# Performance work log

Measured on AMD Instinct MI355X. Metric: run time of the kernel, lower is better.

The kernel has to match this reference:

```python
import jax, jax.numpy as jnp
import numpy as np

EPS = 1e-12
N_WAY, N_SHOT, C_IN, H_IN, W_IN = 5, 5, 640, 24, 24
TOP_LR = 0.8


def _normalize(x, axis):
    # torch F.normalize: x / max(||x||_2, eps)
    n = jnp.sqrt(jnp.sum(x * x, axis=axis, keepdims=True))
    return x / jnp.maximum(n, EPS)


def _conv1x1(x, W, b):
    # x: (B,C,H,W), W: (O,C), b: (O,)
    return jnp.einsum('bchw,oc->bohw', x, W) + b[None, :, None, None]


def _attlayer(x, Wc, bc, Wq, bq, Wk, bk):
    B, C, H, W = x.shape
    HW = H * W
    n_way, n_shot = N_WAY, N_SHOT
    scale = 1.0 / (C ** 0.5)
    x5 = _conv1x1(x, Wc, bc) + x
    x5 = _conv1x1(x5, Wq, bq)            # note: query_transform applied here
    # query_transform applied AGAIN (faithful to original)
    xq = _conv1x1(x5, Wq, bq).reshape(n_way, n_shot, C, HW)
    x_query = jnp.swapaxes(xq, 2, 3).reshape(n_way, n_shot * HW, C)
    xk = _conv1x1(x5, Wk, bk).reshape(n_way, n_shot, C, HW)
    x_key = jnp.swapaxes(xk, 1, 2).reshape(n_way, C, n_shot * HW)
    x_w1 = jnp.matmul(x_query, x_key) * scale          # (n_way, n_shot*HW, n_shot*HW)
    x_w = x_w1.reshape(n_way, n_shot * HW, n_shot, HW).max(-1).mean(-1)
    x_w = jax.nn.softmax(x_w.reshape(n_way, n_shot, HW), axis=-1)
    norm0 = _normalize(x5, 1).reshape(n_way, n_shot, C, H, W)
    # hard-max mask over spatial positions
    mask = (x_w == x_w.max(-1, keepdims=True)).astype(x.dtype)   # (n_way, n_shot, HW)
    seeds = (norm0 * mask.reshape(n_way, n_shot, 1, H, W)).sum((3, 4))  # (n_way, n_shot, C)
    # conv3d with 1x1 spatial kernel over full channel depth == einsum
    cor = jnp.einsum('nkcyx,okc->noyx', norm0, seeds).reshape(n_way, n_shot, HW)
    cmin = cor.min(-1, keepdims=True)
    cmax = cor.max(-1, keepdims=True)
    cor = (cor - cmin) / (cmax - cmin + EPS)
    cormap = cor.reshape(n_way * n_shot, 1, H, W)
    x51 = (x5 * cormap).reshape(n_way, n_shot, C, H, W)
    return x51.mean((1, 3, 4))  # (n_way, C)


def _cdsnet(lf):
    B, C, H, W = lf.shape
    HW = H * W
    n_way, n_shot = N_WAY, N_SHOT
    lfn = _normalize(lf, 1)
    X = jnp.swapaxes(lfn.reshape(B, C, HW), 1, 2)          # (B, HW, C)
    intra = X.reshape(n_way, n_shot * HW, C)
    # d_intra: masked (1-eye) gram mean == (x_i . S_way - ||x_i||^2)/(n_shot*HW)
    S_way = intra.sum(1)                                    # (n_way, C)
    d_intra = (jnp.einsum('nic,nc->ni', intra, S_way) - (intra * intra).sum(-1)) / (n_shot * HW)
    # d_inter: block-diagonal (same-image) pairs masked out
    S_tot = X.sum((0, 1))                                   # (C,)
    S_img = X.sum(1)                                        # (B, C)
    d_inter = (jnp.einsum('bic,c->bi', X, S_tot) - jnp.einsum('bic,bc->bi', X, S_img)) / (B * HW)
    cds = jax.nn.sigmoid(d_intra.reshape(n_way, -1) / d_inter.reshape(n_way, -1))  # (n_way, n_shot*HW)
    k = int(n_shot * HW * TOP_LR)
    _, sel_idx = jax.lax.top_k(cds, k)
    sel = jnp.zeros((n_way, n_shot * HW), lf.dtype)
    sel = sel.at[jnp.arange(n_way)[:, None], sel_idx].set(1.0)
    pos_small = sel.reshape(n_way * n_shot, 1, H, W)
    slf = lf * pos_small                                    # select_local_features
    slf_n = jnp.swapaxes(_normalize(slf.reshape(B, C, HW), 1), 1, 2)
    slf_n = slf_n.reshape(n_way, n_shot, HW, C)
    m1 = slf_n.reshape(n_way, n_shot * HW, C).mean(1)       # (n_way, C)
    l_intra = jnp.matmul(m1, m1.T) * (1.0 - jnp.eye(n_way, dtype=lf.dtype))
    m2 = slf_n.mean(2)                                      # (n_way, n_shot, C)
    l_inter = jnp.einsum('nsc,ntc->nst', m2, m2) * (1.0 - jnp.eye(n_shot, dtype=lf.dtype))
    loss = jnp.exp(l_inter.mean() / l_intra.mean())
    pos_index = jnp.broadcast_to(pos_small, (B, C, H, W))
    neg_index = 1.0 - pos_index
    return loss, pos_index, neg_index


def setup_inputs() -> dict:
    key = jax.random.key(0)
    ks = jax.random.split(key, 7)
    C = C_IN
    s = N_WAY * N_SHOT
    scale = 1.0 / np.sqrt(C)
    lf = jax.random.normal(ks[0], (s, C, H_IN, W_IN), jnp.float32)
    Wc = jax.random.normal(ks[1], (C, C), jnp.float32) * scale
    bc = jax.random.normal(ks[2], (C,), jnp.float32) * 0.01
    Wq = jax.random.normal(ks[3], (C, C), jnp.float32) * scale
    bq = jax.random.normal(ks[4], (C,), jnp.float32) * 0.01
    Wk = jax.random.normal(ks[5], (C, C), jnp.float32) * scale
    bk = jax.random.normal(ks[6], (C,), jnp.float32) * 0.01
    return {'local_feature': lf, 'Wc': Wc, 'bc': bc, 'Wq': Wq, 'bq': bq, 'Wk': Wk, 'bk': bk}


def reference(local_feature, Wc, bc, Wq, bq, Wk, bk):
    s, c, h, w = local_feature.shape
    hw = h * w
    proto1 = _attlayer(local_feature, Wc, bc, Wq, bq, Wk, bk)   # (n_way, C)
    global_proto = jnp.broadcast_to(proto1[:, None, :], (N_WAY, N_SHOT, c)).reshape(s, c)
    gpa = global_proto[:, None, :]                               # (s, 1, C) -> broadcasts to (s, HW, C)
    contrastive_loss, pos_index, neg_index = _cdsnet(local_feature)
    pos_x = _normalize(jnp.swapaxes((local_feature * pos_index).reshape(s, c, hw), 1, 2), -1)
    neg_x = _normalize(jnp.swapaxes((local_feature * neg_index).reshape(s, c, hw), 1, 2), -1)
    pos_value = jnp.exp(pos_x * gpa).sum(-1).mean(-1).mean(-1)
    neg_value = jnp.exp(neg_x * gpa).sum(-1).mean(-1).mean(-1)
    ctc_loss = -jnp.log(pos_value / neg_value)
    return (contrastive_loss, ctc_loss, pos_index)
```

## Files before the change

kernel.cpp:

```cpp
#include <hip/hip_runtime.h>
#include <math.h>

#define NW 5
#define NS 5
#define BB 25
#define CD 640
#define HWD 576
#define NP 2880
#define KTOP 2304
#define EPSF 1e-12f

typedef __attribute__((ext_vector_type(8))) short short8;
typedef __attribute__((ext_vector_type(4))) float f32x4;

__device__ inline unsigned short f2bf(float x) {
    unsigned u = __float_as_uint(x);
    return (unsigned short)((u + 0x7fffu + ((u >> 16) & 1u)) >> 16);
}
__device__ inline float bf2f(unsigned short h) { return __uint_as_float(((unsigned)h) << 16); }

__device__ inline void gload_lds16(const void* g, void* l) {
    __builtin_amdgcn_global_load_lds(
        (const __attribute__((address_space(1))) unsigned int*)g,
        (__attribute__((address_space(3))) unsigned int*)l, 16, 0, 0);
}

__device__ void dev_gemm640(const float* __restrict__ A, const float* __restrict__ B,
                            const float* __restrict__ add, float* __restrict__ C,
                            unsigned short* __restrict__ H, unsigned short* __restrict__ L,
                            int mode, int bx, int by, char* smem)
{
    float (*At)[68] = (float(*)[68])smem;
    float (*Bt)[64] = (float(*)[64])(smem + 8704);
    const int o0 = by * 64, j0 = bx * 64;
    const int t  = threadIdx.x;
    const int to = (t >> 4) * 4, tj = (t & 15) * 4;

    float acc[4][4];
#pragma unroll
    for (int r = 0; r < 4; ++r)
#pragma unroll
        for (int s = 0; s < 4; ++s) acc[r][s] = 0.f;

    for (int c0 = 0; c0 < CD; c0 += 32) {
        __syncthreads();
        {
            const int r = t >> 3, c8 = (t & 7) * 8;
            float4 b0 = *(const float4*)&B[(size_t)(c0+r)*CD + j0 + c8];
            float4 b1 = *(const float4*)&B[(size_t)(c0+r)*CD + j0 + c8 + 4];
            *(float4*)&Bt[r][c8]     = b0;
            *(float4*)&Bt[r][c8 + 4] = b1;
            if (mode == 0) {
                float4 a0 = *(const float4*)&A[(size_t)(c0+r)*CD + o0 + c8];
                float4 a1 = *(const float4*)&A[(size_t)(c0+r)*CD + o0 + c8 + 4];
                *(float4*)&At[r][c8]     = a0;
                *(float4*)&At[r][c8 + 4] = a1;
            } else {
                const int r2 = t >> 2, c82 = (t & 3) * 8;
                float4 a0 = *(const float4*)&A[(size_t)(o0+r2)*CD + c0 + c82];
                float4 a1 = *(const float4*)&A[(size_t)(o0+r2)*CD + c0 + c82 + 4];
                At[c82+0][r2] = a0.x; At[c82+1][r2] = a0.y;
                At[c82+2][r2] = a0.z; At[c82+3][r2] = a0.w;
                At[c82+4][r2] = a1.x; At[c82+5][r2] = a1.y;
                At[c82+6][r2] = a1.z; At[c82+7][r2] = a1.w;
            }
        }
        __syncthreads();
#pragma unroll
        for (int kk = 0; kk < 32; ++kk) {
            float4 av = *(const float4*)&At[kk][to];
            float4 bv = *(const float4*)&Bt[kk][tj];
            float aa[4] = {av.x, av.y, av.z, av.w};
            float bb[4] = {bv.x, bv.y, bv.z, bv.w};
#pragma unroll
            for (int r = 0; r < 4; ++r)
#pragma unroll
                for (int s = 0; s < 4; ++s)
                    acc[r][s] = fmaf(aa[r], bb[s], acc[r][s]);
        }
    }

#pragma unroll
    for (int r = 0; r < 4; ++r) {
        float v[4] = {acc[r][0], acc[r][1], acc[r][2], acc[r][3]};
        const size_t base = (size_t)(o0+to+r)*CD + j0 + tj;
        if (add != nullptr) {
            float4 ad = *(const float4*)&add[base];
            v[0] += ad.x; v[1] += ad.y; v[2] += ad.z; v[3] += ad.w;
        }
        if (C != nullptr) {
            float4 o4; o4.x = v[0]; o4.y = v[1]; o4.z = v[2]; o4.w = v[3];
            *(float4*)&C[base] = o4;
        }
        if (H != nullptr) {
            ushort4 h, l;
            h.x = f2bf(v[0]); h.y = f2bf(v[1]); h.z = f2bf(v[2]); h.w = f2bf(v[3]);
            l.x = f2bf(v[0] - bf2f(h.x)); l.y = f2bf(v[1] - bf2f(h.y));
            l.z = f2bf(v[2] - bf2f(h.z)); l.w = f2bf(v[3] - bf2f(h.w));
            *(ushort4*)&H[base] = h; *(ushort4*)&L[base] = l;
        }
    }
}

__device__ void dev_convert(const float* __restrict__ in, unsigned short* __restrict__ Oh,
                            unsigned short* __restrict__ Ol, int b, int xidx, char* smem)
{
    float (*tile)[65] = (float(*)[65])smem;
    const int c0 = (xidx / 9) * 64;
    const int p0 = (xidx % 9) * 64;
    const int t  = threadIdx.x;
    const float* src = in + (size_t)b * CD * HWD;
#pragma unroll
    for (int it = 0; it < 4; ++it) {
        int cl = (t >> 4) + 16*it, pl = (t & 15) * 4;
        float4 v = *(const float4*)&src[(size_t)(c0+cl)*HWD + p0 + pl];
        tile[cl][pl] = v.x; tile[cl][pl+1] = v.y; tile[cl][pl+2] = v.z; tile[cl][pl+3] = v.w;
    }
    __syncthreads();
#pragma unroll
    for (int it = 0; it < 4; ++it) {
        int pl = (t >> 4) + 16*it, clb = (t & 15) * 4;
        ushort4 hv, lv;
        float x0 = tile[clb+0][pl], x1 = tile[clb+1][pl], x2 = tile[clb+2][pl], x3 = tile[clb+3][pl];
        hv.x = f2bf(x0); hv.y = f2bf(x1); hv.z = f2bf(x2); hv.w = f2bf(x3);
        lv.x = f2bf(x0 - bf2f(hv.x)); lv.y = f2bf(x1 - bf2f(hv.y));
        lv.z = f2bf(x2 - bf2f(hv.z)); lv.w = f2bf(x3 - bf2f(hv.w));
        size_t o = (size_t)(b*HWD + p0 + pl) * CD + c0 + clb;
        *(ushort4*)&Oh[o] = hv;
        *(ushort4*)&Ol[o] = lv;
    }
}

__global__ __launch_bounds__(256) void prep_a(
    const float* __restrict__ lf, const float* __restrict__ Wc,
    const float* __restrict__ bc, const float* __restrict__ Wq,
    const float* __restrict__ bq, const float* __restrict__ Wk,
    const float* __restrict__ bk,
    float* __restrict__ M2, float* __restrict__ Weff,
    float* __restrict__ wqtbk, float* __restrict__ bqwk, float* __restrict__ beff,
    float* __restrict__ sbb,
    unsigned short* __restrict__ lfTh, unsigned short* __restrict__ lfTl,
    float* __restrict__ cor, float* __restrict__ sumsq, float* __restrict__ rvsum,
    float* __restrict__ proto1, float* __restrict__ scal)
{
    __shared__ __align__(16) char smem[16896];
    const int blk = blockIdx.x;
    const int t = threadIdx.x;
    if (blk < 100) {
        dev_gemm640(Wq, Wk, nullptr, M2, nullptr, nullptr, 0, blk % 10, blk / 10, smem);
    } else if (blk < 200) {
        int b2 = blk - 100;
        dev_gemm640(Wq, Wc, Wq, Weff, nullptr, nullptr, 1, b2 % 10, b2 / 10, smem);
    } else if (blk < 210) {
        const int o = (blk - 200)*64 + (t >> 2);
        const int m0 = (t & 3) * 160;
        float s1 = 0.f, s2 = 0.f;
        for (int m = m0; m < m0 + 160; ++m) {
            s1 = fmaf(Wq[(size_t)m*CD + o], bk[m], s1);
            s2 = fmaf(bq[m], Wk[(size_t)m*CD + o], s2);
        }
        s1 += __shfl_xor(s1, 1, 64); s1 += __shfl_xor(s1, 2, 64);
        s2 += __shfl_xor(s2, 1, 64); s2 += __shfl_xor(s2, 2, 64);
        if ((t & 3) == 0) { wqtbk[o] = s1; bqwk[o] = s2; }
    } else if (blk < 220) {
        const int o = (blk - 210)*64 + (t >> 2);
        const int m0 = (t & 3) * 160;
        const float* ap = Wq + (size_t)o*CD + m0;
        float a = 0.f;
        for (int m = 0; m < 160; ++m) a = fmaf(ap[m], bc[m0 + m], a);
        a += __shfl_xor(a, 1, 64); a += __shfl_xor(a, 2, 64);
        if ((t & 3) == 0) beff[o] = a + bq[o];
    } else if (blk == 220) {
        __shared__ float red[4];
        float a = 0.f;
        for (int m = t; m < CD; m += 256) a = fmaf(bq[m], bk[m], a);
        for (int off2 = 32; off2; off2 >>= 1) a += __shfl_down(a, off2, 64);
        if ((t & 63) == 0) red[t >> 6] = a;
        __syncthreads();
        if (t == 0) sbb[0] = red[0] + red[1] + red[2] + red[3];
    } else if (blk < 2471) {
        const int idx = blk - 221;
        dev_convert(lf, lfTh, lfTl, idx / 90, idx % 90, smem);
    } else {
        const int i0 = (blk - 2471)*256 + t;
        for (int i = i0; i < 14400; i += 8192) { cor[i] = 0.f; sumsq[i] = 0.f; rvsum[i] = 0.f; }
        for (int i = i0; i < 3200; i += 8192) proto1[i] = 0.f;
        if (i0 < 2) scal[i0] = 0.f;
    }
}

__global__ __launch_bounds__(256) void prep_b(
    const float* __restrict__ M2, const float* __restrict__ Weff,
    const float* __restrict__ beff, const float* __restrict__ wqtbk,
    unsigned short* __restrict__ WeH, unsigned short* __restrict__ WeL,
    unsigned short* __restrict__ MeH, unsigned short* __restrict__ MeL,
    float* __restrict__ wbias)
{
    __shared__ __align__(16) char smem[16896];
    const int blk = blockIdx.x;
    const int t = threadIdx.x;
    if (blk < 100) {
        dev_gemm640(M2, Weff, nullptr, nullptr, MeH, MeL, 1, blk % 10, blk / 10, smem);
    } else if (blk < 200) {
        int i = (blk - 100)*256 + t;
        float4 v = ((const float4*)Weff)[i];
        ushort4 h, l;
        h.x = f2bf(v.x); h.y = f2bf(v.y); h.z = f2bf(v.z); h.w = f2bf(v.w);
        l.x = f2bf(v.x - bf2f(h.x)); l.y = f2bf(v.y - bf2f(h.y));
        l.z = f2bf(v.z - bf2f(h.z)); l.w = f2bf(v.w - bf2f(h.w));
        ((ushort4*)WeH)[i] = h; ((ushort4*)WeL)[i] = l;
    } else {
        const int o = (blk - 200)*64 + (t >> 2);
        const int m0 = (t & 3) * 160;
        const float* ap = M2 + (size_t)o*CD + m0;
        float a = 0.f;
        for (int m = 0; m < 160; ++m) a = fmaf(ap[m], beff[m0 + m], a);
        a += __shfl_xor(a, 1, 64); a += __shfl_xor(a, 2, 64);
        if ((t & 3) == 0) wbias[o] = a + wqtbk[o];
    }
}

__global__ __launch_bounds__(256) void conv2x(
    const unsigned short* __restrict__ Ah_, const unsigned short* __restrict__ Al_,
    const unsigned short* __restrict__ WeH, const unsigned short* __restrict__ WeL,
    const unsigned short* __restrict__ MeH, const unsigned short* __restrict__ MeL,
    const float* __restrict__ beff, const float* __restrict__ wbias,
    const float* __restrict__ bqwk,
    unsigned short* __restrict__ x5h, unsigned short* __restrict__ x5l,
    unsigned short* __restrict__ wh,  unsigned short* __restrict__ wl,
    float* __restrict__ sumsq, float* __restrict__ rvsum)
{
    __shared__ __align__(16) unsigned short lds[14336];
    const int obx  = blockIdx.x;
    const int osel = (obx < 5);
    const int o0   = (osel ? obx : obx - 5) * 128;
    const unsigned short* Wh = osel ? WeH : MeH;
    const unsigned short* Wl = osel ? WeL : MeL;
    const float* bias = osel ? beff : wbias;
    unsigned short* Oh = osel ? x5h : wh;
    unsigned short* Ol = osel ? x5l : wl;
    const int row0 = blockIdx.y * 96;
    const int t    = threadIdx.x;
    const int w    = t >> 6, lane = t & 63;
    const int ihalf = (w & 1) * 48;
    const int jhalf = (w >> 1) * 64;

    f32x4 acc[3][4];
#pragma unroll
    for (int f = 0; f < 3; ++f)
#pragma unroll
        for (int g = 0; g < 4; ++g) acc[f][g] = (f32x4){0.f,0.f,0.f,0.f};

    const int rl = lane >> 2;
    const int cl = (lane & 3) * 8;

    for (int c0 = 0; c0 < CD; c0 += 32) {
#pragma unroll
        for (int e = 0; e < 7; ++e) {
            const int s = w*7 + e;
            const unsigned short* src;
            if (s < 6)        src = Ah_ + (size_t)(row0 + s*16      + rl)*CD + c0 + cl;
            else if (s < 12)  src = Al_ + (size_t)(row0 + (s-6)*16  + rl)*CD + c0 + cl;
            else if (s < 20)  src = Wh  + (size_t)(o0   + (s-12)*16 + rl)*CD + c0 + cl;
            else              src = Wl  + (size_t)(o0   + (s-20)*16 + rl)*CD + c0 + cl;
            gload_lds16(src, &lds[s*512]);
        }
        __syncthreads();

        const int chunk = (lane >> 4) * 8;
        short8 afh[3], afl[3];
#pragma unroll
        for (int f = 0; f < 3; ++f) {
            int row = ihalf + f*16 + (lane & 15);
            afh[f] = *(const short8*)&lds[row*32 + chunk];
            afl[f] = *(const short8*)&lds[3072 + row*32 + chunk];
        }
#pragma unroll
        for (int g = 0; g < 4; ++g) {
            int row = jhalf + g*16 + (lane & 15);
            short8 bfh = *(const short8*)&lds[6144  + row*32 + chunk];
            short8 bfl = *(const short8*)&lds[10240 + row*32 + chunk];
#pragma unroll
            for (int f = 0; f < 3; ++f) {
                acc[f][g] = __builtin_amdgcn_mfma_f32_16x16x32_bf16(afh[f], bfh, acc[f][g], 0, 0, 0);
                acc[f][g] = __builtin_amdgcn_mfma_f32_16x16x32_bf16(afh[f], bfl, acc[f][g], 0, 0, 0);
                acc[f][g] = __builtin_amdgcn_mfma_f32_16x16x32_bf16(afl[f], bfh, acc[f][g], 0, 0, 0);
            }
        }
        __syncthreads();
    }

    float bs[4], bw[4];
#pragma unroll
    for (int g = 0; g < 4; ++g) {
        const int o = o0 + jhalf + g*16 + (lane & 15);
        bs[g] = bias[o];
        bw[g] = osel ? bqwk[o] : 0.f;
    }
#pragma unroll
    for (int f = 0; f < 3; ++f) {
        const int rbase = row0 + ihalf + f*16 + (lane >> 4)*4;
#pragma unroll
        for (int r = 0; r < 4; ++r) {
            float sq = 0.f, rv = 0.f;
#pragma unroll
            for (int g = 0; g < 4; ++g) {
                const int o = o0 + jhalf + g*16 + (lane & 15);
                const size_t idx = (size_t)(rbase + r)*CD + o;
                float v = acc[f][g][r] + bs[g];
                unsigned short hi = f2bf(v);
                Oh[idx] = hi;
                Ol[idx] = f2bf(v - bf2f(hi));
                sq = fmaf(v, v, sq);
                rv = fmaf(v, bw[g], rv);
            }
            if (osel) {
                sq += __shfl_xor(sq, 1, 64); rv += __shfl_xor(rv, 1, 64);
                sq += __shfl_xor(sq, 2, 64); rv += __shfl_xor(rv, 2, 64);
                sq += __shfl_xor(sq, 4, 64); rv += __shfl_xor(rv, 4, 64);
                sq += __shfl_xor(sq, 8, 64); rv += __shfl_xor(rv, 8, 64);
                if ((lane & 15) == 0) {
                    atomicAdd(&sumsq[rbase + r], sq);
                    atomicAdd(&rvsum[rbase + r], rv);
                }
            }
        }
    }
}

__global__ __launch_bounds__(256) void qk_mfma(
    const unsigned short* __restrict__ Qh, const unsigned short* __restrict__ Ql,
    const unsigned short* __restrict__ Kh, const unsigned short* __restrict__ Kl,
    const float* __restrict__ rvsum, const float* __restrict__ sbb,
    float* __restrict__ xwp)
{
    __shared__ __align__(16) unsigned short lds[18432];
    const int n    = blockIdx.z;
    const int i0   = blockIdx.x * 96;
    const int shot = blockIdx.y / 3;
    const int jt   = blockIdx.y % 3;
    const int t    = threadIdx.x;
    const int w    = t >> 6, lane = t & 63;
    const int ihalf = (w & 1) * 48;
    const int jhalf = (w >> 1) * 96;

    const size_t qbase = (size_t)(n*NP + i0) * CD;
    const size_t kbase = (size_t)(n*NP + shot*HWD + jt*192) * CD;

    f32x4 acc[3][6];
#pragma unroll
    for (int f = 0; f < 3; ++f)
#pragma unroll
        for (int g = 0; g < 6; ++g) acc[f][g] = (f32x4){0.f,0.f,0.f,0.f};

    const int rl = lane >> 2;
    const int cl = (lane & 3) * 8;

    for (int c0 = 0; c0 < CD; c0 += 32) {
#pragma unroll
        for (int e = 0; e < 9; ++e) {
            const int s = w*9 + e;
            const int r = s*16 + rl;
            const unsigned short* src;
            if (s < 6)        src = Qh + qbase + (size_t)r*CD        + c0 + cl;
            else if (s < 12)  src = Ql + qbase + (size_t)(r-96)*CD   + c0 + cl;
            else if (s < 24)  src = Kh + kbase + (size_t)(r-192)*CD  + c0 + cl;
            else              src = Kl + kbase + (size_t)(r-384)*CD  + c0 + cl;
            gload_lds16(src, &lds[s*512]);
        }
        __syncthreads();

        const int chunk = (lane >> 4) * 8;
        short8 afh[3], afl[3];
#pragma unroll
        for (int f = 0; f < 3; ++f) {
            int row = ihalf + f*16 + (lane & 15);
            afh[f] = *(const short8*)&lds[row*32 + chunk];
            afl[f] = *(const short8*)&lds[3072 + row*32 + chunk];
        }
#pragma unroll
        for (int g = 0; g < 6; ++g) {
            int row = jhalf + g*16 + (lane & 15);
            short8 bfh = *(const short8*)&lds[6144  + row*32 + chunk];
            short8 bfl = *(const short8*)&lds[12288 + row*32 + chunk];
#pragma unroll
            for (int f = 0; f < 3; ++f) {
                acc[f][g] = __builtin_amdgcn_mfma_f32_16x16x32_bf16(afh[f], bfh, acc[f][g], 0, 0, 0);
                acc[f][g] = __builtin_amdgcn_mfma_f32_16x16x32_bf16(afh[f], bfl, acc[f][g], 0, 0, 0);
                acc[f][g] = __builtin_amdgcn_mfma_f32_16x16x32_bf16(afl[f], bfh, acc[f][g], 0, 0, 0);
            }
        }
        __syncthreads();
    }

    const float sv = sbb[0];
    float rv[6];
    {
        int jg0 = n*NP + shot*HWD + jt*192 + jhalf + (lane & 15);
#pragma unroll
        for (int g = 0; g < 6; ++g) rv[g] = rvsum[jg0 + g*16] + sv;
    }
    float* smax = (float*)lds;
#pragma unroll
    for (int f = 0; f < 3; ++f) {
#pragma unroll
        for (int r = 0; r < 4; ++r) {
            float m = -INFINITY;
#pragma unroll
            for (int g = 0; g < 6; ++g) m = fmaxf(m, acc[f][g][r] + rv[g]);
#pragma unroll
            for (int off = 1; off < 16; off <<= 1) m = fmaxf(m, __shfl_xor(m, off, 64));
            if ((lane & 15) == 0) smax[(ihalf + f*16 + (lane >> 4)*4 + r)*2 + (w >> 1)] = m;
        }
    }
    __syncthreads();
    if (t < 96) {
        float m = fmaxf(smax[t*2], smax[t*2 + 1]);
        xwp[(((size_t)n*5 + shot)*3 + jt)*NP + i0 + t] = m;
    }
}

__global__ __launch_bounds__(640) void post_a(
    const float* __restrict__ lf, const float* __restrict__ xwp,
    const unsigned short* __restrict__ Xh, const unsigned short* __restrict__ Xl,
    const float* __restrict__ sumsq, float* __restrict__ invnl,
    float* __restrict__ seeds)
{
    const int blk = blockIdx.x;
    const int t = threadIdx.x;
    if (blk < 90) {
        const int pg = blk*160 + (t >> 2);
        const int cb = (t & 3) * 160;
        const int b = pg / HWD, p = pg - (pg / HWD) * HWD;
        const float* sp = lf + (size_t)b*CD*HWD + (size_t)cb*HWD + p;
        float a = 0.f;
        for (int c = 0; c < 160; ++c) { float v = sp[(size_t)c*HWD]; a = fmaf(v, v, a); }
        a += __shfl_xor(a, 1, 64); a += __shfl_xor(a, 2, 64);
        if ((t & 3) == 0) invnl[pg] = 1.f / fmaxf(sqrtf(a), EPSF);
        return;
    }
    const int b = blk - 90;
    const int n = b / NS, sq = b % NS;
    __shared__ float wv[9]; __shared__ int wi[9]; __shared__ int spix;
    if (t < 576) {
        const int i = sq * HWD + t;
        float v = 0.f;
#pragma unroll
        for (int s = 0; s < NS; ++s) {
            float m = -INFINITY;
#pragma unroll
            for (int tt = 0; tt < 3; ++tt)
                m = fmaxf(m, xwp[(((size_t)(n*NS+s))*3 + tt)*NP + i]);
            v += m;
        }
        int lane = t & 63, w = t >> 6;
        float bv = v; int bi = t;
        for (int off = 32; off; off >>= 1) {
            float ov = __shfl_down(bv, off, 64);
            int   oi = __shfl_down(bi, off, 64);
            if (ov > bv || (ov == bv && oi < bi)) { bv = ov; bi = oi; }
        }
        if (lane == 0) { wv[w] = bv; wi[w] = bi; }
    }
    __syncthreads();
    if (t == 0) {
        float best = wv[0]; int bidx = wi[0];
        for (int k = 1; k < 9; ++k)
            if (wv[k] > best || (wv[k] == best && wi[k] < bidx)) { best = wv[k]; bidx = wi[k]; }
        spix = bidx;
    }
    __syncthreads();
    const int row = b*HWD + spix;
    const float in1 = 1.f / fmaxf(sqrtf(sumsq[row]), EPSF);
    float v = bf2f(Xh[(size_t)row*CD + t]) + bf2f(Xl[(size_t)row*CD + t]);
    seeds[b*CD + t] = v * in1;
}

__global__ __launch_bounds__(256) void post_b(
    const unsigned short* __restrict__ Xh, const unsigned short* __restrict__ Xl,
    const float* __restrict__ sumsq, const float* __restrict__ seeds,
    const float* __restrict__ lf, const float* __restrict__ invnl,
    float* __restrict__ cor, float* __restrict__ S_img)
{
    const int blk = blockIdx.x;
    const int t = threadIdx.x;
    if (blk < 900) {
        const int zc = blk / 225, rem = blk % 225;
        const int pb = rem % 9, b = rem / 9;
        const int n = b / NS, k = b % NS;
        const int p = pb*64 + (t >> 2);
        const int row = b*HWD + p;
        const int cb = zc*160 + (t & 3) * 40;
        const unsigned short* ph = Xh + (size_t)row*CD + cb;
        const unsigned short* pl = Xl + (size_t)row*CD + cb;
        float a[5] = {0.f,0.f,0.f,0.f,0.f};
        for (int c = 0; c < 40; c += 8) {
            short8 h8 = *(const short8*)&ph[c];
            short8 l8 = *(const short8*)&pl[c];
#pragma unroll
            for (int j = 0; j < 8; ++j) {
                float v = bf2f((unsigned short)h8[j]) + bf2f((unsigned short)l8[j]);
#pragma unroll
                for (int o = 0; o < 5; ++o)
                    a[o] = fmaf(v, seeds[(o*NS + k)*CD + cb + c + j], a[o]);
            }
        }
        const float in1 = 1.f / fmaxf(sqrtf(sumsq[row]), EPSF);
#pragma unroll
        for (int o = 0; o < 5; ++o) {
            float s = a[o];
            s += __shfl_xor(s, 1, 64); s += __shfl_xor(s, 2, 64);
            if ((t & 3) == 0) atomicAdd(&cor[(n*5 + o)*HWD + p], in1 * s);
        }
        return;
    }
    const int i = blk - 900;
    const int ct = i % 160, b = i / 160;
    const int pi = t & 63, cj = t >> 6;
    const int c = ct * 4 + cj;
    const float* xp = lf + ((size_t)b * CD + c) * HWD;
    const float* ip = invnl + b * HWD;
    float acc = 0.f;
    for (int p = pi; p < HWD; p += 64) acc = fmaf(xp[p], ip[p], acc);
    for (int off = 32; off; off >>= 1) acc += __shfl_down(acc, off, 64);
    if (pi == 0) S_img[b * CD + c] = acc;
}

__global__ __launch_bounds__(256) void post_c(
    const unsigned short* __restrict__ Xh, const unsigned short* __restrict__ Xl,
    const float* __restrict__ cor, const float* __restrict__ S_img,
    float* __restrict__ proto1, float* __restrict__ S_way, float* __restrict__ S_tot)
{
    const int blk = blockIdx.x;
    const int t = threadIdx.x;
    if (blk < 200) {
        __shared__ float corb[NP];
        __shared__ float sacc[256];
        __shared__ float mnv[5], mxv[5];
        const int n = blk / 40, rem = blk % 40;
        const int ct = rem % 10, rch = rem / 10;
        for (int j = t; j < NP; j += 256) corb[j] = cor[n*NP + j];
        __syncthreads();
        {
            const int lane = t & 63;
            for (int o = t >> 6; o < 5; o += 4) {
                float mn = INFINITY, mx = -INFINITY;
                for (int j = lane; j < HWD; j += 64) {
                    float v = corb[o*HWD + j];
                    mn = fminf(mn, v); mx = fmaxf(mx, v);
                }
                for (int off = 32; off; off >>= 1) {
                    mn = fminf(mn, __shfl_xor(mn, off, 64));
                    mx = fmaxf(mx, __shfl_xor(mx, off, 64));
                }
                if (lane == 0) { mnv[o] = mn; mxv[o] = mx; }
            }
        }
        __syncthreads();
        for (int j = t; j < NP; j += 256) {
            int o = j / HWD;
            corb[j] = (corb[j] - mnv[o]) / (mxv[o] - mnv[o] + EPSF);
        }
        __syncthreads();
        const int c = ct*64 + (t & 63);
        const int rc = t >> 6;
        const int r0 = rch*720 + rc*180;
        float a = 0.f;
        for (int rr = r0; rr < r0 + 180; ++rr) {
            size_t row = (size_t)(n*NP + rr);
            float v = bf2f(Xh[row*CD + c]) + bf2f(Xl[row*CD + c]);
            a = fmaf(v, corb[rr], a);
        }
        sacc[t] = a;
        __syncthreads();
        if (t < 64) {
            float s = sacc[t] + sacc[t+64] + sacc[t+128] + sacc[t+192];
            atomicAdd(&proto1[n*CD + c], s * (1.f / 2880.f));
        }
        return;
    }
    for (int c = t; c < CD; c += 256) {
        float tot = 0.f;
        for (int nn = 0; nn < NW; ++nn) {
            float w = 0.f;
            for (int s = 0; s < NS; ++s) w += S_img[(nn*NS+s)*CD + c];
            S_way[nn*CD + c] = w; tot += w;
        }
        S_tot[c] = tot;
    }
}

__global__ __launch_bounds__(256) void cds_v2(const float* __restrict__ lf, const float* __restrict__ invn,
                           const float* __restrict__ S_way, const float* __restrict__ S_img,
                           const float* __restrict__ S_tot, float* __restrict__ cds)
{
    const int b = blockIdx.y, t = threadIdx.x;
    const int p = blockIdx.x*64 + (t >> 2);
    const int cb = (t & 3) * 160;
    const int n = b / NS;
    const float* xp = lf + (size_t)b*CD*HWD + p + (size_t)cb*HWD;
    const float* wv = S_way + n*CD + cb;
    const float* iv = S_img + b*CD + cb;
    const float* tv = S_tot + cb;
    float dw = 0.f, di = 0.f, dt = 0.f, sq = 0.f;
    for (int c = 0; c < 160; ++c) {
        float v = xp[(size_t)c*HWD];
        dw = fmaf(v, wv[c], dw);
        di = fmaf(v, iv[c], di);
        dt = fmaf(v, tv[c], dt);
        sq = fmaf(v, v, sq);
    }
    dw += __shfl_xor(dw,1,64); dw += __shfl_xor(dw,2,64);
    di += __shfl_xor(di,1,64); di += __shfl_xor(di,2,64);
    dt += __shfl_xor(dt,1,64); dt += __shfl_xor(dt,2,64);
    sq += __shfl_xor(sq,1,64); sq += __shfl_xor(sq,2,64);
    if ((t & 3) == 0) {
        float in1 = invn[b*HWD + p];
        float d_intra = (in1 * dw - in1 * in1 * sq) * (1.f / 2880.f);
        float d_inter = (in1 * dt - in1 * di) * (1.f / 14400.f);
        float r = d_intra / d_inter;
        cds[n * NP + (b % NS) * HWD + p] = 1.f / (1.f + expf(-r));
    }
}

__global__ void topk_kernel(const float* __restrict__ cds, float* __restrict__ sel)
{
    __shared__ unsigned int u[NP];
    __shared__ int hist[256];
    __shared__ int red[16];
    __shared__ int bcast;
    __shared__ unsigned sprefix;
    __shared__ int skk;
    __shared__ int scanbuf[576];
    const int n = blockIdx.x, t = threadIdx.x;
    for (int j = t; j < NP; j += 576) {
        unsigned int x = __float_as_uint(cds[n * NP + j]);
        u[j] = (x & 0x80000000u) ? ~x : (x | 0x80000000u);
    }
    if (t == 0) { skk = KTOP; sprefix = 0u; }
    __syncthreads();
    const int j0 = t * 5;
    for (int byte = 3; byte >= 0; --byte) {
        if (t < 256) hist[t] = 0;
        __syncthreads();
        const int sh = byte * 8;
        const unsigned pmask = (byte == 3) ? 0u : (0xFFFFFFFFu << (sh + 8));
        const unsigned pref = sprefix;
#pragma unroll
        for (int e = 0; e < 5; ++e) {
            unsigned v = u[j0+e];
            if ((v & pmask) == pref) atomicAdd(&hist[(v >> sh) & 255], 1);
        }
        __syncthreads();
        if (t == 0) {
            int kk = skk, acc = 0, b2;
            for (b2 = 255; b2 >= 0; --b2) { acc += hist[b2]; if (acc >= kk) break; }
            skk = kk - (acc - hist[b2]);
            sprefix = pref | ((unsigned)b2 << sh);
        }
        __syncthreads();
    }
    const unsigned int T = sprefix;
    int cg = 0, ce = 0;
#pragma unroll
    for (int e = 0; e < 5; ++e) {
        unsigned v = u[j0+e];
        if (v > T) cg++; else if (v == T) ce++;
    }
    const int lane = t & 63, w = t >> 6;
    int r1 = cg;
    for (int off = 32; off; off >>= 1) r1 += __shfl_down(r1, off, 64);
    if (lane == 0) red[w] = r1;
    __syncthreads();
    if (t == 0) { int s2 = 0; for (int q = 0; q < 9; ++q) s2 += red[q]; bcast = s2; }
    __syncthreads();
    const int need = KTOP - bcast;
    scanbuf[t] = ce;
    __syncthreads();
    for (int off = 1; off < 576; off <<= 1) {
        int v2 = (t >= off) ? scanbuf[t - off] : 0;
        __syncthreads();
        scanbuf[t] += v2;
        __syncthreads();
    }
    int excl = scanbuf[t] - ce;
    int eidx = 0;
#pragma unroll
    for (int e = 0; e < 5; ++e) {
        int j = j0 + e;
        unsigned v = u[j];
        float s = 0.f;
        if (v > T) s = 1.f;
        else if (v == T) { if (excl + eidx < need) s = 1.f; eidx++; }
        int sh2 = j / HWD;
        sel[(n*NS + sh2) * HWD + (j - sh2*HWD)] = s;
    }
}

__global__ __launch_bounds__(256) void post_d(
    const float* __restrict__ lf, const float* __restrict__ invnl,
    const float* __restrict__ sel, const float* __restrict__ proto1,
    float* __restrict__ Sm, float* __restrict__ scal)
{
    const int blk = blockIdx.x;
    const int t = threadIdx.x;
    if (blk < 4000) {
        const int ct = blk % 160, b = blk / 160;
        const int pi = t & 63, cj = t >> 6;
        const int c = ct * 4 + cj;
        const float* xp = lf + ((size_t)b * CD + c) * HWD;
        const float* ip = invnl + b * HWD;
        const float* mp = sel + b * HWD;
        float acc = 0.f;
        for (int p = pi; p < HWD; p += 64) acc = fmaf(xp[p], ip[p] * mp[p], acc);
        for (int off = 32; off; off >>= 1) acc += __shfl_down(acc, off, 64);
        if (pi == 0) Sm[b * CD + c] = acc;
        return;
    }
    const int i = blk - 4000;
    const int pb = i % 9, b = i / 9;
    const int p = pb*64 + (t >> 2);
    const int cb = (t & 3) * 160;
    const int n = b / NS;
    const float* xp = lf + (size_t)b*CD*HWD + p + (size_t)cb*HWD;
    const float* pr = proto1 + n*CD + cb;
    float in1 = invnl[b*HWD + p];
    float acc = 0.f;
    for (int c = 0; c < 160; ++c) acc += expf(xp[(size_t)c*HWD] * in1 * pr[c]);
    acc += __shfl_xor(acc, 1, 64); acc += __shfl_xor(acc, 2, 64);
    float pv = 0.f, nv = 0.f;
    if ((t & 3) == 0) {
        float s = sel[b*HWD + p];
        pv = (s > 0.5f) ? acc : 640.f;
        nv = (s > 0.5f) ? 640.f : acc;
    }
    for (int off = 32; off >= 4; off >>= 1) {
        pv += __shfl_down(pv, off, 64);
        nv += __shfl_down(nv, off, 64);
    }
    if ((t & 63) == 0) { atomicAdd(&scal[0], pv); atomicAdd(&scal[1], nv); }
}

__global__ __launch_bounds__(256) void fin_kernel(
    const float* __restrict__ sel, const float* __restrict__ Sm,
    const float* __restrict__ scal, float* __restrict__ out)
{
    const int blk = blockIdx.x;
    const int t = threadIdx.x;
    if (blk < 9000) {
        int idx = blk * 256 + t;
        int row = idx / 144;
        int f4  = idx - row * 144;
        int b   = row / CD;
        const float* sp = sel + b * HWD + f4 * 4;
        float* op = out + 2 + (size_t)row * HWD + f4 * 4;
        float2 v0 = make_float2(sp[0], sp[1]);
        float2 v1 = make_float2(sp[2], sp[3]);
        *(float2*)op = v0; *(float2*)(op + 2) = v1;
        return;
    }
    if (blk == 9001) {
        if (t == 0) out[1] = -(logf(scal[0]) - logf(scal[1]));
        return;
    }
    __shared__ double sa[4], sb2[4], sc[4];
    double A = 0.0, Bv = 0.0, Cv = 0.0;
    for (int c = t; c < CD; c += 256) {
        float tot = 0.f;
        for (int nn = 0; nn < NW; ++nn) {
            float ws = 0.f;
            for (int s = 0; s < NS; ++s) {
                float v = Sm[(nn*NS+s)*CD + c];
                ws += v; Cv += (double)v * v;
            }
            tot += ws; A += (double)ws * ws;
        }
        Bv += (double)tot * tot;
    }
    const int lane = t & 63, w = t >> 6;
    for (int off = 32; off; off >>= 1) {
        A  += __shfl_down(A,  off, 64);
        Bv += __shfl_down(Bv, off, 64);
        Cv += __shfl_down(Cv, off, 64);
    }
    if (lane == 0) { sa[w] = A; sb2[w] = Bv; sc[w] = Cv; }
    __syncthreads();
    if (t == 0) {
        double a = 0, b2 = 0, cc = 0;
        for (int q = 0; q < 4; ++q) { a += sa[q]; b2 += sb2[q]; cc += sc[q]; }
        out[0] = (float)exp(5.0 * (a - cc) / (b2 - a));
    }
}

extern "C" void kernel_launch(void* const* d_in, const int* in_sizes, int n_in,
                              void* d_out, int out_size, void* d_ws, size_t ws_size,
                              hipStream_t stream) {
    const float* lf = (const float*)d_in[0];
    const float* Wc = (const float*)d_in[1];
    const float* bc = (const float*)d_in[2];
    const float* Wq = (const float*)d_in[3];
    const float* bq = (const float*)d_in[4];
    const float* Wk = (const float*)d_in[5];
    const float* bk = (const float*)d_in[6];
    float* out = (float*)d_out;
    float* ws = (float*)d_ws;

    const size_t FEAT = 9216000;
    size_t off = 0;
    auto alloc = [&](size_t nf) { float* p = ws + off; off += (nf + 3) & ~(size_t)3; return p; };
    float* s0     = alloc(FEAT);
    float* s1     = alloc(FEAT);
    float* xwp    = alloc(216000);
    float* seeds  = alloc(16000);
    float* invnl  = alloc(14400);
    float* sumsq  = alloc(14400);
    float* rvsum  = alloc(14400);
    float* cor    = alloc(14400);
    float* proto1 = alloc(3200);
    float* S_img  = alloc(16000);
    float* S_way  = alloc(3200);
    float* S_tot  = alloc(640);
    float* cds    = alloc(14400);
    float* sel    = alloc(14400);
    float* Sm     = alloc(16000);
    float* scal   = alloc(8);
    float* wqtbk  = alloc(640);
    float* bqwk   = alloc(640);
    float* sbb    = alloc(4);
    float* beff   = alloc(640);
    float* wbias  = alloc(640);
    float* WeS    = alloc(409600);
    float* MeS    = alloc(409600);

    float* M2   = s1;
    float* Weff = s1 + 409600;

    unsigned short* WeH = (unsigned short*)WeS; unsigned short* WeL = WeH + 409600;
    unsigned short* MeH = (unsigned short*)MeS; unsigned short* MeL = MeH + 409600;

    unsigned short* lfTh = (unsigned short*)(out + 2);
    unsigned short* lfTl = lfTh + FEAT;

    unsigned short* s0h = (unsigned short*)s0; unsigned short* s0l = s0h + FEAT;
    unsigned short* s1h = (unsigned short*)s1; unsigned short* s1l = s1h + FEAT;

    prep_a<<<2503, 256, 0, stream>>>(lf, Wc, bc, Wq, bq, Wk, bk,
                                     M2, Weff, wqtbk, bqwk, beff, sbb,
                                     lfTh, lfTl, cor, sumsq, rvsum, proto1, scal);
    prep_b<<<210, 256, 0, stream>>>(M2, Weff, beff, wqtbk, WeH, WeL, MeH, MeL, wbias);
    conv2x<<<dim3(10,150), 256, 0, stream>>>(lfTh, lfTl, WeH, WeL, MeH, MeL,
                                             beff, wbias, bqwk,
                                             s0h, s0l, s1h, s1l, sumsq, rvsum);
    qk_mfma<<<dim3(30,15,5), 256, 0, stream>>>(s0h, s0l, s1h, s1l, rvsum, sbb, xwp);
    post_a<<<115, 640, 0, stream>>>(lf, xwp, s0h, s0l, sumsq, invnl, seeds);
    post_b<<<4900, 256, 0, stream>>>(s0h, s0l, sumsq, seeds, lf, invnl, cor, S_img);
    post_c<<<201, 256, 0, stream>>>(s0h, s0l, cor, S_img, proto1, S_way, S_tot);
    cds_v2<<<dim3(9,25), 256, 0, stream>>>(lf, invnl, S_way, S_img, S_tot, cds);
    topk_kernel<<<5, 576, 0, stream>>>(cds, sel);
    post_d<<<4225, 256, 0, stream>>>(lf, invnl, sel, proto1, Sm, scal);
    fin_kernel<<<9002, 256, 0, stream>>>(sel, Sm, scal, out);
}
```

Measured before the change: 709.3 us.

## Compute two output tiles per conv2x block and fold pos_index broadcast into post_d

```diff
diff --git a/kernel.cpp b/kernel.cpp
--- a/kernel.cpp
+++ b/kernel.cpp
@@ -230,39 +230,44 @@
     unsigned short* __restrict__ wh,  unsigned short* __restrict__ wl,
     float* __restrict__ sumsq, float* __restrict__ rvsum)
 {
-    __shared__ __align__(16) unsigned short lds[14336];
-    const int obx  = blockIdx.x;
-    const int osel = (obx < 5);
-    const int o0   = (osel ? obx : obx - 5) * 128;
-    const unsigned short* Wh = osel ? WeH : MeH;
-    const unsigned short* Wl = osel ? WeL : MeL;
-    const float* bias = osel ? beff : wbias;
-    unsigned short* Oh = osel ? x5h : wh;
-    unsigned short* Ol = osel ? x5l : wl;
+    __shared__ __align__(16) unsigned short lds[22528];
     const int row0 = blockIdx.y * 96;
     const int t    = threadIdx.x;
     const int w    = t >> 6, lane = t & 63;
     const int ihalf = (w & 1) * 48;
     const int jhalf = (w >> 1) * 64;
 
-    f32x4 acc[3][4];
-#pragma unroll
-    for (int f = 0; f < 3; ++f)
-#pragma unroll
-        for (int g = 0; g < 4; ++g) acc[f][g] = (f32x4){0.f,0.f,0.f,0.f};
+    const int tile0 = blockIdx.x * 2;
+    const int tile1 = tile0 + 1;
+    const int osel0 = (tile0 < 5), osel1 = (tile1 < 5);
+    const int o00 = (tile0 % 5) * 128, o01 = (tile1 % 5) * 128;
+    const unsigned short* W0h = osel0 ? WeH : MeH;
+    const unsigned short* W0l = osel0 ? WeL : MeL;
+    const unsigned short* W1h = osel1 ? WeH : MeH;
+    const unsigned short* W1l = osel1 ? WeL : MeL;
+
+    f32x4 acc[2][3][4];
+#pragma unroll
+    for (int ot = 0; ot < 2; ++ot)
+#pragma unroll
+        for (int f = 0; f < 3; ++f)
+#pragma unroll
+            for (int g = 0; g < 4; ++g) acc[ot][f][g] = (f32x4){0.f,0.f,0.f,0.f};
 
     const int rl = lane >> 2;
     const int cl = (lane & 3) * 8;
 
     for (int c0 = 0; c0 < CD; c0 += 32) {
 #pragma unroll
-        for (int e = 0; e < 7; ++e) {
-            const int s = w*7 + e;
+        for (int e = 0; e < 11; ++e) {
+            const int s = w*11 + e;
             const unsigned short* src;
             if (s < 6)        src = Ah_ + (size_t)(row0 + s*16      + rl)*CD + c0 + cl;
             else if (s < 12)  src = Al_ + (size_t)(row0 + (s-6)*16  + rl)*CD + c0 + cl;
-            else if (s < 20)  src = Wh  + (size_t)(o0   + (s-12)*16 + rl)*CD + c0 + cl;
-            else              src = Wl  + (size_t)(o0   + (s-20)*16 + rl)*CD + c0 + cl;
+            else if (s < 20)  src = W0h + (size_t)(o00  + (s-12)*16 + rl)*CD + c0 + cl;
+            else if (s < 28)  src = W0l + (size_t)(o00  + (s-20)*16 + rl)*CD + c0 + cl;
+            else if (s < 36)  src = W1h + (size_t)(o01  + (s-28)*16 + rl)*CD + c0 + cl;
+            else              src = W1l + (size_t)(o01  + (s-36)*16 + rl)*CD + c0 + cl;
             gload_lds16(src, &lds[s*512]);
         }
         __syncthreads();
@@ -276,52 +281,65 @@
             afl[f] = *(const short8*)&lds[3072 + row*32 + chunk];
         }
 #pragma unroll
+        for (int ot = 0; ot < 2; ++ot) {
+            const int bh = 6144 + ot*8192;
+            const int bl = bh + 4096;
+#pragma unroll
+            for (int g = 0; g < 4; ++g) {
+                int row = jhalf + g*16 + (lane & 15);
+                short8 bfh = *(const short8*)&lds[bh + row*32 + chunk];
+                short8 bfl = *(const short8*)&lds[bl + row*32 + chunk];
+#pragma unroll
+                for (int f = 0; f < 3; ++f) {
+                    acc[ot][f][g] = __builtin_amdgcn_mfma_f32_16x16x32_bf16(afh[f], bfh, acc[ot][f][g], 0, 0, 0);
+                    acc[ot][f][g] = __builtin_amdgcn_mfma_f32_16x16x32_bf16(afh[f], bfl, acc[ot][f][g], 0, 0, 0);
+                    acc[ot][f][g] = __builtin_amdgcn_mfma_f32_16x16x32_bf16(afl[f], bfh, acc[ot][f][g], 0, 0, 0);
+                }
+            }
+        }
+        __syncthreads();
+    }
+
+#pragma unroll
+    for (int ot = 0; ot < 2; ++ot) {
+        const int osel = ot ? osel1 : osel0;
+        const int o0   = ot ? o01 : o00;
+        const float* bias = osel ? beff : wbias;
+        unsigned short* Oh = osel ? x5h : wh;
+        unsigned short* Ol = osel ? x5l : wl;
+        float bs[4], bw[4];
+#pragma unroll
         for (int g = 0; g < 4; ++g) {
-            int row = jhalf + g*16 + (lane & 15);
-            short8 bfh = *(const short8*)&lds[6144  + row*32 + chunk];
-            short8 bfl = *(const short8*)&lds[10240 + row*32 + chunk];
-#pragma unroll
-            for (int f = 0; f < 3; ++f) {
-                acc[f][g] = __builtin_amdgcn_mfma_f32_16x16x32_bf16(afh[f], bfh, acc[f][g], 0, 0, 0);
-                acc[f][g] = __builtin_amdgcn_mfma_f32_16x16x32_bf16(afh[f], bfl, acc[f][g], 0, 0, 0);
-                acc[f][g] = __builtin_amdgcn_mfma_f32_16x16x32_bf16(afl[f], bfh, acc[f][g], 0, 0, 0);
-            }
-        }
-        __syncthreads();
-    }
-
-    float bs[4], bw[4];
-#pragma unroll
-    for (int g = 0; g < 4; ++g) {
-        const int o = o0 + jhalf + g*16 + (lane & 15);
-        bs[g] = bias[o];
-        bw[g] = osel ? bqwk[o] : 0.f;
-    }
-#pragma unroll
-    for (int f = 0; f < 3; ++f) {
-        const int rbase = row0 + ihalf + f*16 + (lane >> 4)*4;
-#pragma unroll
-        for (int r = 0; r < 4; ++r) {
-            float sq = 0.f, rv = 0.f;
-#pragma unroll
-            for (int g = 0; g < 4; ++g) {
-                const int o = o0 + jhalf + g*16 + (lane & 15);
-                const size_t idx = (size_t)(rbase + r)*CD + o;
-                float v = acc[f][g][r] + bs[g];
-                unsigned short hi = f2bf(v);
-                Oh[idx] = hi;
-                Ol[idx] = f2bf(v - bf2f(hi));
-                sq = fmaf(v, v, sq);
-                rv = fmaf(v, bw[g], rv);
-            }
-            if (osel) {
-                sq += __shfl_xor(sq, 1, 64); rv += __shfl_xor(rv, 1, 64);
-                sq += __shfl_xor(sq, 2, 64); rv += __shfl_xor(rv, 2, 64);
-                sq += __shfl_xor(sq, 4, 64); rv += __shfl_xor(rv, 4, 64);
-                sq += __shfl_xor(sq, 8, 64); rv += __shfl_xor(rv, 8, 64);
-                if ((lane & 15) == 0) {
-                    atomicAdd(&sumsq[rbase + r], sq);
-                    atomicAdd(&rvsum[rbase + r], rv);
+            const int o = o0 + jhalf + g*16 + (lane & 15);
+            bs[g] = bias[o];
+            bw[g] = osel ? bqwk[o] : 0.f;
+        }
+#pragma unroll
+        for (int f = 0; f < 3; ++f) {
+            const int rbase = row0 + ihalf + f*16 + (lane >> 4)*4;
+#pragma unroll
+            for (int r = 0; r < 4; ++r) {
+                float sq = 0.f, rv = 0.f;
+#pragma unroll
+                for (int g = 0; g < 4; ++g) {
+                    const int o = o0 + jhalf + g*16 + (lane & 15);
+                    const size_t idx = (size_t)(rbase + r)*CD + o;
+                    float v = acc[ot][f][g][r] + bs[g];
+                    unsigned short hi = f2bf(v);
+                    Oh[idx] = hi;
+                    Ol[idx] = f2bf(v - bf2f(hi));
+                    sq = fmaf(v, v, sq);
+                    rv = fmaf(v, bw[g], rv);
+                }
+                if (osel) {
+                    sq += __shfl_xor(sq, 1, 64); rv += __shfl_xor(rv, 1, 64);
+                    sq += __shfl_xor(sq, 2, 64); rv += __shfl_xor(rv, 2, 64);
+                    sq += __shfl_xor(sq, 4, 64); rv += __shfl_xor(rv, 4, 64);
+                    sq += __shfl_xor(sq, 8, 64); rv += __shfl_xor(rv, 8, 64);
+                    if ((lane & 15) == 0) {
+                        atomicAdd(&sumsq[rbase + r], sq);
+                        atomicAdd(&rvsum[rbase + r], rv);
+                    }
                 }
             }
         }
@@ -700,7 +718,7 @@
 __global__ __launch_bounds__(256) void post_d(
     const float* __restrict__ lf, const float* __restrict__ invnl,
     const float* __restrict__ sel, const float* __restrict__ proto1,
-    float* __restrict__ Sm, float* __restrict__ scal)
+    float* __restrict__ Sm, float* __restrict__ scal, float* __restrict__ out)
 {
     const int blk = blockIdx.x;
     const int t = threadIdx.x;
@@ -717,49 +735,49 @@
         if (pi == 0) Sm[b * CD + c] = acc;
         return;
     }
-    const int i = blk - 4000;
-    const int pb = i % 9, b = i / 9;
-    const int p = pb*64 + (t >> 2);
-    const int cb = (t & 3) * 160;
-    const int n = b / NS;
-    const float* xp = lf + (size_t)b*CD*HWD + p + (size_t)cb*HWD;
-    const float* pr = proto1 + n*CD + cb;
-    float in1 = invnl[b*HWD + p];
-    float acc = 0.f;
-    for (int c = 0; c < 160; ++c) acc += expf(xp[(size_t)c*HWD] * in1 * pr[c]);
-    acc += __shfl_xor(acc, 1, 64); acc += __shfl_xor(acc, 2, 64);
-    float pv = 0.f, nv = 0.f;
-    if ((t & 3) == 0) {
-        float s = sel[b*HWD + p];
-        pv = (s > 0.5f) ? acc : 640.f;
-        nv = (s > 0.5f) ? 640.f : acc;
-    }
-    for (int off = 32; off >= 4; off >>= 1) {
-        pv += __shfl_down(pv, off, 64);
-        nv += __shfl_down(nv, off, 64);
-    }
-    if ((t & 63) == 0) { atomicAdd(&scal[0], pv); atomicAdd(&scal[1], nv); }
+    if (blk < 4225) {
+        const int i = blk - 4000;
+        const int pb = i % 9, b = i / 9;
+        const int p = pb*64 + (t >> 2);
+        const int cb = (t & 3) * 160;
+        const int n = b / NS;
+        const float* xp = lf + (size_t)b*CD*HWD + p + (size_t)cb*HWD;
+        const float* pr = proto1 + n*CD + cb;
+        float in1 = invnl[b*HWD + p];
+        float acc = 0.f;
+        for (int c = 0; c < 160; ++c) acc += expf(xp[(size_t)c*HWD] * in1 * pr[c]);
+        acc += __shfl_xor(acc, 1, 64); acc += __shfl_xor(acc, 2, 64);
+        float pv = 0.f, nv = 0.f;
+        if ((t & 3) == 0) {
+            float s = sel[b*HWD + p];
+            pv = (s > 0.5f) ? acc : 640.f;
+            nv = (s > 0.5f) ? 640.f : acc;
+        }
+        for (int off = 32; off >= 4; off >>= 1) {
+            pv += __shfl_down(pv, off, 64);
+            nv += __shfl_down(nv, off, 64);
+        }
+        if ((t & 63) == 0) { atomicAdd(&scal[0], pv); atomicAdd(&scal[1], nv); }
+        return;
+    }
+    int idx = (blk - 4225) * 256 + t;
+    int row = idx / 144;
+    int f4  = idx - row * 144;
+    int b   = row / CD;
+    const float* sp = sel + b * HWD + f4 * 4;
+    float* op = out + 2 + (size_t)row * HWD + f4 * 4;
+    float2 v0 = make_float2(sp[0], sp[1]);
+    float2 v1 = make_float2(sp[2], sp[3]);
+    *(float2*)op = v0; *(float2*)(op + 2) = v1;
 }
 
 __global__ __launch_bounds__(256) void fin_kernel(
-    const float* __restrict__ sel, const float* __restrict__ Sm,
-    const float* __restrict__ scal, float* __restrict__ out)
+    const float* __restrict__ Sm, const float* __restrict__ scal,
+    float* __restrict__ out)
 {
     const int blk = blockIdx.x;
     const int t = threadIdx.x;
-    if (blk < 9000) {
-        int idx = blk * 256 + t;
-        int row = idx / 144;
-        int f4  = idx - row * 144;
-        int b   = row / CD;
-        const float* sp = sel + b * HWD + f4 * 4;
-        float* op = out + 2 + (size_t)row * HWD + f4 * 4;
-        float2 v0 = make_float2(sp[0], sp[1]);
-        float2 v1 = make_float2(sp[2], sp[3]);
-        *(float2*)op = v0; *(float2*)(op + 2) = v1;
-        return;
-    }
-    if (blk == 9001) {
+    if (blk == 1) {
         if (t == 0) out[1] = -(logf(scal[0]) - logf(scal[1]));
         return;
     }
@@ -848,15 +866,15 @@
                                      M2, Weff, wqtbk, bqwk, beff, sbb,
                                      lfTh, lfTl, cor, sumsq, rvsum, proto1, scal);
     prep_b<<<210, 256, 0, stream>>>(M2, Weff, beff, wqtbk, WeH, WeL, MeH, MeL, wbias);
-    conv2x<<<dim3(10,150), 256, 0, stream>>>(lfTh, lfTl, WeH, WeL, MeH, MeL,
-                                             beff, wbias, bqwk,
-                                             s0h, s0l, s1h, s1l, sumsq, rvsum);
+    conv2x<<<dim3(5,150), 256, 0, stream>>>(lfTh, lfTl, WeH, WeL, MeH, MeL,
+                                            beff, wbias, bqwk,
+                                            s0h, s0l, s1h, s1l, sumsq, rvsum);
     qk_mfma<<<dim3(30,15,5), 256, 0, stream>>>(s0h, s0l, s1h, s1l, rvsum, sbb, xwp);
     post_a<<<115, 640, 0, stream>>>(lf, xwp, s0h, s0l, sumsq, invnl, seeds);
     post_b<<<4900, 256, 0, stream>>>(s0h, s0l, sumsq, seeds, lf, invnl, cor, S_img);
     post_c<<<201, 256, 0, stream>>>(s0h, s0l, cor, S_img, proto1, S_way, S_tot);
     cds_v2<<<dim3(9,25), 256, 0, stream>>>(lf, invnl, S_way, S_img, S_tot, cds);
     topk_kernel<<<5, 576, 0, stream>>>(cds, sel);
-    post_d<<<4225, 256, 0, stream>>>(lf, invnl, sel, proto1, Sm, scal);
-    fin_kernel<<<9002, 256, 0, stream>>>(sel, Sm, scal, out);
-}
+    post_d<<<13225, 256, 0, stream>>>(lf, invnl, sel, proto1, Sm, scal, out);
+    fin_kernel<<<2, 256, 0, stream>>>(Sm, scal, out);
+}
```

After: 731.8 us. +3.2%, slower.
